# Kernel optimization log

Hardware: AMD Instinct MI355X
Metric: run time of the kernel (lower is better)

The kernel has to match this reference:

```python
import jax, jax.numpy as jnp
import numpy as np

D_MODEL = 2048
N_HEADS = 16
N_KV_HEADS = 4
D_K = D_MODEL // N_HEADS          # 128
N_REP = N_HEADS // N_KV_HEADS     # 4
MAX_SEQ_LEN = 2048


def _rope_tables():
    # Matches torch Rotary: d_k//4 geometric freqs followed by d_k//4 zeros.
    freqs = (1.0 / 10000.0) ** jnp.linspace(0.0, 1.0, D_K // 4, dtype=jnp.float32)
    freqs = jnp.concatenate([freqs, jnp.zeros(D_K // 4, dtype=jnp.float32)])
    t = jnp.arange(MAX_SEQ_LEN, dtype=jnp.float32)
    theta = t[:, None] * freqs[None, :]          # [max_seq_len, d_k//2]
    return jnp.cos(theta), jnp.sin(theta)


def _apply_rotary(x, cos, sin):
    # Faithful to original: x is (B, H, T, D) and the table is indexed by
    # x.size(-3) == H (the original code rotates per-HEAD, broadcast over time).
    H = x.shape[1]
    c = cos[None, :H, None, :]
    s = sin[None, :H, None, :]
    xf = x.astype(jnp.float32)
    x1, x2 = jnp.split(xf, 2, axis=-1)
    y1 = x1 * c + x2 * s
    y2 = -x1 * s + x2 * c
    return jnp.concatenate([y1, y2], axis=-1).astype(x.dtype)


def setup_inputs() -> dict:
    key = jax.random.key(0)
    ks = jax.random.split(key, 5)
    B, T = 2, 2048
    scale = 1.0 / np.sqrt(D_MODEL)
    x = jax.random.normal(ks[0], (B, T, D_MODEL), dtype=jnp.float32)
    wq = jax.random.normal(ks[1], (N_HEADS * D_K, D_MODEL), dtype=jnp.float32) * scale
    wk = jax.random.normal(ks[2], (N_KV_HEADS * D_K, D_MODEL), dtype=jnp.float32) * scale
    wv = jax.random.normal(ks[3], (N_KV_HEADS * D_K, D_MODEL), dtype=jnp.float32) * scale
    wo = jax.random.normal(ks[4], (D_MODEL, D_MODEL), dtype=jnp.float32) * scale
    return {"x": x, "wq": wq, "wk": wk, "wv": wv, "wo": wo}


def reference(x, wq, wk, wv, wo):
    B, T, _ = x.shape
    cos, sin = _rope_tables()

    Q = (x @ wq.T).reshape(B, T, N_HEADS, D_K).transpose(0, 2, 1, 3)      # (B,Hq,T,D)
    K = (x @ wk.T).reshape(B, T, N_KV_HEADS, D_K).transpose(0, 2, 1, 3)   # (B,Hkv,T,D)
    V = (x @ wv.T).reshape(B, T, N_KV_HEADS, D_K).transpose(0, 2, 1, 3)

    Q = _apply_rotary(Q, cos, sin)
    K = _apply_rotary(K, cos, sin)

    # repeat_interleave over head dim to match query heads
    K = jnp.repeat(K, N_REP, axis=1)   # (B,Hq,T,D)
    V = jnp.repeat(V, N_REP, axis=1)

    scale = 1.0 / jnp.sqrt(jnp.asarray(D_K, dtype=jnp.float32))
    scores = jnp.einsum('bhqd,bhkd->bhqk', Q, K) * scale
    causal = jnp.tril(jnp.ones((T, T), dtype=bool))
    scores = jnp.where(causal[None, None, :, :], scores, jnp.finfo(scores.dtype).min)
    attn = jax.nn.softmax(scores, axis=-1)
    out = jnp.einsum('bhqk,bhkd->bhqd', attn, V)          # (B,Hq,T,D)
    out = out.transpose(0, 2, 1, 3).reshape(B, T, D_MODEL)
    return out @ wo.T
```

## Files before the change

kernel.cpp:

```cpp
#include <hip/hip_runtime.h>
#include <cstdint>
#include <cstddef>

typedef __attribute__((ext_vector_type(8))) short bf16x8;
typedef __attribute__((ext_vector_type(4))) float f32x4;
typedef __attribute__((ext_vector_type(16))) float f32x16;
typedef unsigned short ushort_t;

#define MFMA_BF16(a, b, c) __builtin_amdgcn_mfma_f32_16x16x32_bf16((a), (b), (c), 0, 0, 0)
#define MFMA32_BF16(a, b, c) __builtin_amdgcn_mfma_f32_32x32x16_bf16((a), (b), (c), 0, 0, 0)

__device__ __forceinline__ unsigned short f2bf(float f) {
  unsigned int u = __float_as_uint(f);
  u += 0x7fffu + ((u >> 16) & 1u);
  return (unsigned short)(u >> 16);
}
__device__ __forceinline__ float bf2f(unsigned short h) {
  return __uint_as_float(((unsigned int)h) << 16);
}
__device__ __forceinline__ float exp2_fast(float x) {
  float r;
  asm("v_exp_f32 %0, %1" : "=v"(r) : "v"(x));
  return r;
}
__device__ __forceinline__ uint32_t cvtpk_bf16(float lo, float hi) {
  uint32_t r;
  asm("v_cvt_pk_bf16_f32 %0, %1, %2" : "=v"(r) : "v"(lo), "v"(hi));
  return r;
}

__device__ __forceinline__ void gload_lds16(const void* g, void* lds) {
  __builtin_amdgcn_global_load_lds(
      (const __attribute__((address_space(1))) void*)g,
      (__attribute__((address_space(3))) void*)lds, 16, 0, 0);
}

__global__ __launch_bounds__(256)
void cvt_kernel(const float* __restrict__ x, const float* __restrict__ wq,
                const float* __restrict__ wk, const float* __restrict__ wv,
                const float* __restrict__ wo,
                ushort_t* __restrict__ xb, ushort_t* __restrict__ wqb,
                ushort_t* __restrict__ wkb, ushort_t* __restrict__ wvb,
                ushort_t* __restrict__ wob) {
  const float* src; ushort_t* dst; int n;
  switch (blockIdx.y) {
    case 0:  src = x;  dst = xb;  n = 8388608; break;
    case 1:  src = wq; dst = wqb; n = 4194304; break;
    case 2:  src = wk; dst = wkb; n = 1048576; break;
    case 3:  src = wv; dst = wvb; n = 1048576; break;
    default: src = wo; dst = wob; n = 4194304; break;
  }
  const int i = (int)(blockIdx.x * 256u + threadIdx.x) * 4;
  if (i >= n) return;
  const float4 v = *(const float4*)(src + i);
  union { unsigned short us[4]; unsigned long long u64; } pk;
  pk.us[0] = f2bf(v.x); pk.us[1] = f2bf(v.y);
  pk.us[2] = f2bf(v.z); pk.us[3] = f2bf(v.w);
  *(unsigned long long*)(dst + i) = pk.u64;
}

__global__ __launch_bounds__(256, 2)
void gemm_qkv(const ushort_t* __restrict__ A,
              const ushort_t* __restrict__ WQ, const ushort_t* __restrict__ WK,
              const ushort_t* __restrict__ WV,
              ushort_t* __restrict__ Qb, ushort_t* __restrict__ Kb,
              ushort_t* __restrict__ Vtb) {
  __shared__ bf16x8 smem_v[4096];
  char* smem = (char*)smem_v;
  const int tid  = threadIdx.x;
  const int lane = tid & 63;
  const int wave = tid >> 6;
  const int wr = wave >> 1, wc = wave & 1;
  const int y = blockIdx.y;
  int mode, ylocal;
  const ushort_t* Bsel;
  if (y < 16)      { mode = 0; ylocal = y;      Bsel = WQ; }
  else if (y < 20) { mode = 1; ylocal = y - 16; Bsel = WK; }
  else             { mode = 2; ylocal = y - 20; Bsel = WV; }
  const ushort_t* Abase = A + (size_t)blockIdx.x * 128 * 2048;
  const ushort_t* Bbase = Bsel + (size_t)ylocal * 128 * 2048;

  f32x4 acc[4][4] = {};

  #pragma unroll
  for (int it = 0; it < 4; ++it) {
    const int chunk = it * 4 + wave;
    const int r  = chunk * 8 + (lane >> 3);
    const int cg = (lane & 7) ^ (r & 7);
    gload_lds16(Abase + (size_t)r * 2048 + cg * 8, smem + chunk * 1024);
    gload_lds16(Bbase + (size_t)r * 2048 + cg * 8, smem + 16384 + chunk * 1024);
  }
  __syncthreads();

  for (int t = 0; t < 32; ++t) {
    if (t + 1 < 32) {
      char* dst = smem + ((t + 1) & 1) * 32768;
      const int k0 = (t + 1) * 64;
      #pragma unroll
      for (int it = 0; it < 4; ++it) {
        const int chunk = it * 4 + wave;
        const int r  = chunk * 8 + (lane >> 3);
        const int cg = (lane & 7) ^ (r & 7);
        gload_lds16(Abase + (size_t)r * 2048 + k0 + cg * 8, dst + chunk * 1024);
        gload_lds16(Bbase + (size_t)r * 2048 + k0 + cg * 8, dst + 16384 + chunk * 1024);
      }
    }

    char* As = smem + (t & 1) * 32768;
    char* Bs = As + 16384;
    bf16x8 af[2][4], bf_[2][4];
    #pragma unroll
    for (int kki = 0; kki < 2; ++kki) {
      #pragma unroll
      for (int m = 0; m < 4; ++m) {
        const int row = wr * 64 + m * 16 + (lane & 15);
        const int cg  = ((kki << 2) + (lane >> 4)) ^ (row & 7);
        af[kki][m] = *(const bf16x8*)(As + row * 128 + cg * 16);
      }
      #pragma unroll
      for (int n = 0; n < 4; ++n) {
        const int row = wc * 64 + n * 16 + (lane & 15);
        const int cg  = ((kki << 2) + (lane >> 4)) ^ (row & 7);
        bf_[kki][n] = *(const bf16x8*)(Bs + row * 128 + cg * 16);
      }
    }
    #pragma unroll
    for (int kki = 0; kki < 2; ++kki)
      #pragma unroll
      for (int m = 0; m < 4; ++m)
        #pragma unroll
        for (int n = 0; n < 4; ++n)
          acc[m][n] = MFMA_BF16(af[kki][m], bf_[kki][n], acc[m][n]);

    __syncthreads();
  }

  const int row0 = blockIdx.x * 128 + wr * 64;
  const int col0 = ylocal * 128 + wc * 64;
  #pragma unroll
  for (int m = 0; m < 4; ++m) {
    #pragma unroll
    for (int n = 0; n < 4; ++n) {
      #pragma unroll
      for (int j = 0; j < 4; ++j) {
        const int gm = row0 + m * 16 + ((lane >> 4) << 2) + j;
        const int gn = col0 + n * 16 + (lane & 15);
        const float v = acc[m][n][j];
        if (mode == 0) {
          Qb[(size_t)gm * 2048 + gn] = f2bf(v);
        } else if (mode == 1) {
          Kb[(size_t)gm * 512 + gn] = f2bf(v);
        } else {
          const int bb = gm >> 11, t2 = gm & 2047;
          Vtb[(size_t)bb * 512 * 2048 + (size_t)gn * 2048 + t2] = f2bf(v);
        }
      }
    }
  }
}

template<int WMODE>
__global__ __launch_bounds__(256, 2)
void gemm_bt(const ushort_t* __restrict__ A, const ushort_t* __restrict__ B,
             void* __restrict__ Cout, int M, int N, int K) {
  __shared__ bf16x8 smem_v[4096];
  char* smem = (char*)smem_v;
  const int tid  = threadIdx.x;
  const int lane = tid & 63;
  const int wave = tid >> 6;
  const int wr = wave >> 1, wc = wave & 1;
  const ushort_t* Abase = A + (size_t)blockIdx.x * 128 * K;
  const ushort_t* Bbase = B + (size_t)blockIdx.y * 128 * K;

  f32x4 acc[4][4] = {};
  const int nk = K >> 6;

  #pragma unroll
  for (int it = 0; it < 4; ++it) {
    const int chunk = it * 4 + wave;
    const int r  = chunk * 8 + (lane >> 3);
    const int cg = (lane & 7) ^ (r & 7);
    gload_lds16(Abase + (size_t)r * K + cg * 8, smem + chunk * 1024);
    gload_lds16(Bbase + (size_t)r * K + cg * 8, smem + 16384 + chunk * 1024);
  }
  __syncthreads();

  for (int t = 0; t < nk; ++t) {
    if (t + 1 < nk) {
      char* dst = smem + ((t + 1) & 1) * 32768;
      const int k0 = (t + 1) * 64;
      #pragma unroll
      for (int it = 0; it < 4; ++it) {
        const int chunk = it * 4 + wave;
        const int r  = chunk * 8 + (lane >> 3);
        const int cg = (lane & 7) ^ (r & 7);
        gload_lds16(Abase + (size_t)r * K + k0 + cg * 8, dst + chunk * 1024);
        gload_lds16(Bbase + (size_t)r * K + k0 + cg * 8, dst + 16384 + chunk * 1024);
      }
    }

    char* As = smem + (t & 1) * 32768;
    char* Bs = As + 16384;
    bf16x8 af[2][4], bf_[2][4];
    #pragma unroll
    for (int kki = 0; kki < 2; ++kki) {
      #pragma unroll
      for (int m = 0; m < 4; ++m) {
        const int row = wr * 64 + m * 16 + (lane & 15);
        const int cg  = ((kki << 2) + (lane >> 4)) ^ (row & 7);
        af[kki][m] = *(const bf16x8*)(As + row * 128 + cg * 16);
      }
      #pragma unroll
      for (int n = 0; n < 4; ++n) {
        const int row = wc * 64 + n * 16 + (lane & 15);
        const int cg  = ((kki << 2) + (lane >> 4)) ^ (row & 7);
        bf_[kki][n] = *(const bf16x8*)(Bs + row * 128 + cg * 16);
      }
    }
    #pragma unroll
    for (int kki = 0; kki < 2; ++kki)
      #pragma unroll
      for (int m = 0; m < 4; ++m)
        #pragma unroll
        for (int n = 0; n < 4; ++n)
          acc[m][n] = MFMA_BF16(af[kki][m], bf_[kki][n], acc[m][n]);

    __syncthreads();
  }

  const int row0 = blockIdx.x * 128 + wr * 64;
  const int col0 = blockIdx.y * 128 + wc * 64;
  #pragma unroll
  for (int m = 0; m < 4; ++m) {
    #pragma unroll
    for (int n = 0; n < 4; ++n) {
      #pragma unroll
      for (int j = 0; j < 4; ++j) {
        const int gm = row0 + m * 16 + ((lane >> 4) << 2) + j;
        const int gn = col0 + n * 16 + (lane & 15);
        const float v = acc[m][n][j];
        if (WMODE == 0) {
          ((ushort_t*)Cout)[(size_t)gm * N + gn] = f2bf(v);
        } else if (WMODE == 1) {
          ((float*)Cout)[(size_t)gm * N + gn] = v;
        } else {
          const int bb = gm >> 11, t2 = gm & 2047;
          ((ushort_t*)Cout)[(size_t)bb * N * 2048 + (size_t)gn * 2048 + t2] = f2bf(v);
        }
      }
    }
  }
}

__global__ __launch_bounds__(256)
void rope_k_kernel(ushort_t* __restrict__ K) {
  const int idx = blockIdx.x * 256 + threadIdx.x;
  const int NK = 4096 * 4 * 32;
  if (idx >= NK) return;
  const int t = idx >> 7, r = idx & 127;
  const int h = r >> 5, i = r & 31;
  ushort_t* p = K + (size_t)t * 512 + h * 128;
  const float f  = powf(10000.0f, -(float)i / 31.0f);
  const float th = (float)h * f;
  float sn, cs;
  sincosf(th, &sn, &cs);
  const float x1 = bf2f(p[i]), x2 = bf2f(p[i + 64]);
  p[i]      = f2bf(x1 * cs + x2 * sn);
  p[i + 64] = f2bf(-x1 * sn + x2 * cs);
}

__global__ __launch_bounds__(256, 2)
void attn_kernel(const ushort_t* __restrict__ Q, const ushort_t* __restrict__ K,
                 const ushort_t* __restrict__ Vt, ushort_t* __restrict__ AO) {
  __shared__ bf16x8 smem_v[4096];
  char* smem = (char*)smem_v;
  const int tid  = threadIdx.x;
  const int lane = tid & 63;
  const int wq   = tid >> 6;
  const int ql   = lane & 31;
  const int hi   = lane >> 5;
  const int h  = blockIdx.y;
  const int b  = blockIdx.z;
  const int qt = (b == 0) ? ((int)gridDim.x - 1 - (int)blockIdx.x)
                          : (int)blockIdx.x;
  const int kh = h >> 2;
  const int q0b = qt * 128;
  const int qmin_w = q0b + wq * 32;
  const int qmax_w = qmin_w + 31;
  const int qrow = qmin_w + ql;

  const ushort_t* Qp = Q  + (size_t)b * 2048 * 2048 + (size_t)h  * 128;
  const ushort_t* Kp = K  + (size_t)b * 2048 * 512  + (size_t)kh * 128;
  const ushort_t* Vp = Vt + (size_t)b * 512 * 2048  + (size_t)kh * 128 * 2048;

  const int ntiles = (qt + 1) * 2;

  #pragma unroll
  for (int it = 0; it < 4; ++it) {
    const int ck = it * 4 + wq;
    const int rK = ck * 4 + (lane >> 4);
    const int gK = (lane & 15) ^ (rK & 7);
    gload_lds16(Kp + (size_t)rK * 512 + gK * 8, smem + ck * 1024);
    const int rV = ck * 8 + (lane >> 3);
    const int gV = (lane & 7) ^ (rV & 7);
    gload_lds16(Vp + (size_t)rV * 2048 + gV * 8, smem + 16384 + ck * 1024);
  }

  const float SCL = 0.08838834764831845f * 1.4426950408889634f;
  bf16x8 qf[8];
  #pragma unroll
  for (int ks = 0; ks < 8; ++ks)
    qf[ks] = *(const bf16x8*)(Qp + (size_t)qrow * 2048 + ks * 16 + hi * 8);
  #pragma unroll
  for (int ks = 0; ks < 2; ++ks) {
    union { bf16x8 v; ushort_t us[8]; } X1, X2;
    X1.v = qf[ks]; X2.v = qf[ks + 4];
    #pragma unroll
    for (int e = 0; e < 8; ++e) {
      const int i = ks * 16 + hi * 8 + e;
      const float f = __expf(-(float)i * (9.2103403720f / 31.0f));
      float sn, cs;
      sincosf((float)h * f, &sn, &cs);
      const float x1 = bf2f(X1.us[e]), x2 = bf2f(X2.us[e]);
      X1.us[e] = f2bf((x1 * cs + x2 * sn) * SCL);
      X2.us[e] = f2bf((-x1 * sn + x2 * cs) * SCL);
    }
    qf[ks] = X1.v; qf[ks + 4] = X2.v;
  }
  #pragma unroll
  for (int ks = 2; ks < 4; ++ks) {
    union { bf16x8 v; ushort_t us[8]; } X1, X2;
    X1.v = qf[ks]; X2.v = qf[ks + 4];
    #pragma unroll
    for (int e = 0; e < 8; ++e) {
      X1.us[e] = f2bf(bf2f(X1.us[e]) * SCL);
      X2.us[e] = f2bf(bf2f(X2.us[e]) * SCL);
    }
    qf[ks] = X1.v; qf[ks + 4] = X2.v;
  }

  float m_ = -3.0e38f, l_ = 0.f;
  f32x16 oacc[4] = {};

  __syncthreads();

  for (int ti = 0; ti < ntiles; ++ti) {
    const int kv0 = ti * 64;
    if (ti + 1 < ntiles) {
      const int nkv0 = kv0 + 64;
      char* dst = smem + ((ti + 1) & 1) * 32768;
      #pragma unroll
      for (int it = 0; it < 4; ++it) {
        const int ck = it * 4 + wq;
        const int rK = ck * 4 + (lane >> 4);
        const int gK = (lane & 15) ^ (rK & 7);
        gload_lds16(Kp + (size_t)(nkv0 + rK) * 512 + gK * 8, dst + ck * 1024);
        const int rV = ck * 8 + (lane >> 3);
        const int gV = (lane & 7) ^ (rV & 7);
        gload_lds16(Vp + (size_t)rV * 2048 + nkv0 + gV * 8, dst + 16384 + ck * 1024);
      }
    }

    char* Ks = smem + (ti & 1) * 32768;
    char* Vs = Ks + 16384;
    if (kv0 <= qmax_w) {
      f32x16 sacc[2] = {};
      __builtin_amdgcn_s_setprio(1);
      #pragma unroll
      for (int kg = 0; kg < 2; ++kg) {
        const int key = kg * 32 + ql;
        #pragma unroll
        for (int ks = 0; ks < 8; ++ks) {
          const int g = ((ks << 1) + hi) ^ (key & 7);
          const bf16x8 kf = *(const bf16x8*)(Ks + key * 256 + g * 16);
          sacc[kg] = MFMA32_BF16(kf, qf[ks], sacc[kg]);
        }
      }
      __builtin_amdgcn_s_setprio(0);

      if (kv0 + 63 > qmin_w) {
        #pragma unroll
        for (int kg = 0; kg < 2; ++kg)
          #pragma unroll
          for (int r = 0; r < 16; ++r) {
            const int keyg = kv0 + kg * 32 + (r & 3) + 8 * (r >> 2) + 4 * hi;
            if (keyg > qrow) sacc[kg][r] = -3.0e38f;
          }
      }

      float mx[8];
      #pragma unroll
      for (int i = 0; i < 8; ++i) {
        const int kg = i >> 2, base = (i & 3) * 4;
        mx[i] = fmaxf(fmaxf(sacc[kg][base], sacc[kg][base + 1]),
                      fmaxf(sacc[kg][base + 2], sacc[kg][base + 3]));
      }
      float pm = fmaxf(fmaxf(fmaxf(mx[0], mx[1]), fmaxf(mx[2], mx[3])),
                       fmaxf(fmaxf(mx[4], mx[5]), fmaxf(mx[6], mx[7])));
      pm = fmaxf(pm, __shfl_xor(pm, 32));

      if (__any(pm > m_ + 11.0f)) {
        const float mn = fmaxf(m_, pm);
        const float alpha = exp2_fast(m_ - mn);
        m_ = mn;
        l_ *= alpha;
        #pragma unroll
        for (int r = 0; r < 16; ++r) {
          const float ar = __shfl(alpha, (r & 3) + 8 * (r >> 2) + 4 * hi);
          #pragma unroll
          for (int dg = 0; dg < 4; ++dg) oacc[dg][r] *= ar;
        }
      }

      float rs0 = 0.f, rs1 = 0.f, rs2 = 0.f, rs3 = 0.f;
      #pragma unroll
      for (int kg = 0; kg < 2; ++kg)
        #pragma unroll
        for (int r = 0; r < 16; r += 4) {
          const float p0 = exp2_fast(sacc[kg][r]     - m_);
          const float p1 = exp2_fast(sacc[kg][r + 1] - m_);
          const float p2 = exp2_fast(sacc[kg][r + 2] - m_);
          const float p3 = exp2_fast(sacc[kg][r + 3] - m_);
          sacc[kg][r] = p0; sacc[kg][r + 1] = p1;
          sacc[kg][r + 2] = p2; sacc[kg][r + 3] = p3;
          rs0 += p0; rs1 += p1; rs2 += p2; rs3 += p3;
        }
      float rs = (rs0 + rs1) + (rs2 + rs3);
      rs += __shfl_xor(rs, 32);
      l_ += rs;

      bf16x8 pa[4];
      #pragma unroll
      for (int ks = 0; ks < 4; ++ks) {
        const int kg = ks >> 1;
        const int base = 8 * (ks & 1);
        union { uint32_t w[4]; bf16x8 v; } U;
        #pragma unroll
        for (int j = 0; j < 2; ++j) {
          uint32_t a  = cvtpk_bf16(sacc[kg][base + 2 * j],     sacc[kg][base + 2 * j + 1]);
          uint32_t bb = cvtpk_bf16(sacc[kg][base + 4 + 2 * j], sacc[kg][base + 4 + 2 * j + 1]);
          asm volatile("v_permlane32_swap_b32 %0, %1" : "+v"(a), "+v"(bb));
          U.w[j] = a; U.w[2 + j] = bb;
        }
        pa[ks] = U.v;
      }

      __builtin_amdgcn_s_setprio(1);
      #pragma unroll
      for (int dg = 0; dg < 4; ++dg) {
        const int d = dg * 32 + ql;
        #pragma unroll
        for (int ks = 0; ks < 4; ++ks) {
          const int g = ((ks << 1) + hi) ^ (d & 7);
          const bf16x8 vf = *(const bf16x8*)(Vs + d * 128 + g * 16);
          oacc[dg] = MFMA32_BF16(pa[ks], vf, oacc[dg]);
        }
      }
      __builtin_amdgcn_s_setprio(0);
    }

    __syncthreads();
  }

  const float linv = 1.0f / l_;
  ushort_t* AOp = AO + (size_t)b * 2048 * 2048 + (size_t)h * 128;
  #pragma unroll
  for (int r = 0; r < 16; ++r) {
    const int cr = (r & 3) + 8 * (r >> 2) + 4 * hi;
    const float li = __shfl(linv, cr);
    const int row = q0b + wq * 32 + cr;
    #pragma unroll
    for (int dg = 0; dg < 4; ++dg)
      AOp[(size_t)row * 2048 + dg * 32 + ql] = f2bf(oacc[dg][r] * li);
  }
}

extern "C" void kernel_launch(void* const* d_in, const int* in_sizes, int n_in,
                              void* d_out, int out_size, void* d_ws, size_t ws_size,
                              hipStream_t stream) {
  const float* x  = (const float*)d_in[0];
  const float* wq = (const float*)d_in[1];
  const float* wk = (const float*)d_in[2];
  const float* wv = (const float*)d_in[3];
  const float* wo = (const float*)d_in[4];
  float* out = (float*)d_out;
  char* ws = (char*)d_ws;

  ushort_t* xb  = (ushort_t*)(ws);
  ushort_t* wqb = (ushort_t*)(ws + 16777216);
  ushort_t* wkb = (ushort_t*)(ws + 25165824);
  ushort_t* wvb = (ushort_t*)(ws + 27262976);
  ushort_t* wob = (ushort_t*)(ws + 29360128);
  ushort_t* Qb  = (ushort_t*)(ws + 37748736);
  ushort_t* Kb  = (ushort_t*)(ws + 54525952);
  ushort_t* Vtb = (ushort_t*)(ws + 58720256);
  ushort_t* AOb = (ushort_t*)(ws + 62914560);

  cvt_kernel<<<dim3(8192, 5), 256, 0, stream>>>(x, wq, wk, wv, wo,
                                                xb, wqb, wkb, wvb, wob);
  gemm_qkv<<<dim3(32, 24), 256, 0, stream>>>(xb, wqb, wkb, wvb, Qb, Kb, Vtb);
  rope_k_kernel<<<dim3(2048), 256, 0, stream>>>(Kb);
  attn_kernel<<<dim3(16, 16, 2), 256, 0, stream>>>(Qb, Kb, Vtb, AOb);
  gemm_bt<1><<<dim3(32, 16), 256, 0, stream>>>(AOb, wob, out, 4096, 2048, 2048);
}
```

Measured before the change: 189.9 us.

## Halve QKV GEMM K-tile for higher occupancy and remap attention blocks per XCD

The QKV projection GEMM now stages 32-wide K slices instead of 64. This halves its shared memory to 32 KB and allows 3 blocks per CU, with a new swizzle matched to the narrower rows. The cost is twice as many loop iterations and barriers. Separately, the attention grid index is remapped so blocks that share a KV head and batch land on the same XCD, aiming for better L2 reuse of K/V. The remap also pairs causal query tiles (qt and 15-qt) for load balance.

```diff
diff --git a/kernel.cpp b/kernel.cpp
--- a/kernel.cpp
+++ b/kernel.cpp
@@ -59,13 +59,13 @@
   *(unsigned long long*)(dst + i) = pk.u64;
 }
 
-__global__ __launch_bounds__(256, 2)
+__global__ __launch_bounds__(256, 3)
 void gemm_qkv(const ushort_t* __restrict__ A,
               const ushort_t* __restrict__ WQ, const ushort_t* __restrict__ WK,
               const ushort_t* __restrict__ WV,
               ushort_t* __restrict__ Qb, ushort_t* __restrict__ Kb,
               ushort_t* __restrict__ Vtb) {
-  __shared__ bf16x8 smem_v[4096];
+  __shared__ bf16x8 smem_v[2048];
   char* smem = (char*)smem_v;
   const int tid  = threadIdx.x;
   const int lane = tid & 63;
@@ -82,58 +82,52 @@
 
   f32x4 acc[4][4] = {};
 
-  #pragma unroll
-  for (int it = 0; it < 4; ++it) {
-    const int chunk = it * 4 + wave;
-    const int r  = chunk * 8 + (lane >> 3);
-    const int cg = (lane & 7) ^ (r & 7);
-    gload_lds16(Abase + (size_t)r * 2048 + cg * 8, smem + chunk * 1024);
-    gload_lds16(Bbase + (size_t)r * 2048 + cg * 8, smem + 16384 + chunk * 1024);
-  }
+#define QKV_STAGE(T, BUF)                                                    \
+  {                                                                          \
+    const int k0_ = (T) * 32;                                                \
+    _Pragma("unroll")                                                        \
+    for (int it = 0; it < 2; ++it) {                                         \
+      const int c = it * 4 + wave;                                           \
+      const int row = c * 16 + (lane >> 2);                                  \
+      const int gs = (lane & 3) ^ ((row >> 1) & 3);                          \
+      gload_lds16(Abase + (size_t)row * 2048 + k0_ + gs * 8, (BUF) + c * 1024);       \
+      gload_lds16(Bbase + (size_t)row * 2048 + k0_ + gs * 8, (BUF) + 8192 + c * 1024);\
+    }                                                                        \
+  }
+
+  QKV_STAGE(0, smem);
   __syncthreads();
 
-  for (int t = 0; t < 32; ++t) {
-    if (t + 1 < 32) {
-      char* dst = smem + ((t + 1) & 1) * 32768;
-      const int k0 = (t + 1) * 64;
-      #pragma unroll
-      for (int it = 0; it < 4; ++it) {
-        const int chunk = it * 4 + wave;
-        const int r  = chunk * 8 + (lane >> 3);
-        const int cg = (lane & 7) ^ (r & 7);
-        gload_lds16(Abase + (size_t)r * 2048 + k0 + cg * 8, dst + chunk * 1024);
-        gload_lds16(Bbase + (size_t)r * 2048 + k0 + cg * 8, dst + 16384 + chunk * 1024);
-      }
-    }
-
-    char* As = smem + (t & 1) * 32768;
-    char* Bs = As + 16384;
-    bf16x8 af[2][4], bf_[2][4];
-    #pragma unroll
-    for (int kki = 0; kki < 2; ++kki) {
-      #pragma unroll
-      for (int m = 0; m < 4; ++m) {
-        const int row = wr * 64 + m * 16 + (lane & 15);
-        const int cg  = ((kki << 2) + (lane >> 4)) ^ (row & 7);
-        af[kki][m] = *(const bf16x8*)(As + row * 128 + cg * 16);
-      }
-      #pragma unroll
-      for (int n = 0; n < 4; ++n) {
-        const int row = wc * 64 + n * 16 + (lane & 15);
-        const int cg  = ((kki << 2) + (lane >> 4)) ^ (row & 7);
-        bf_[kki][n] = *(const bf16x8*)(Bs + row * 128 + cg * 16);
-      }
-    }
-    #pragma unroll
-    for (int kki = 0; kki < 2; ++kki)
-      #pragma unroll
-      for (int m = 0; m < 4; ++m)
-        #pragma unroll
-        for (int n = 0; n < 4; ++n)
-          acc[m][n] = MFMA_BF16(af[kki][m], bf_[kki][n], acc[m][n]);
+  for (int t = 0; t < 64; ++t) {
+    if (t + 1 < 64) {
+      char* dst = smem + ((t + 1) & 1) * 16384;
+      QKV_STAGE(t + 1, dst);
+    }
+
+    char* As = smem + (t & 1) * 16384;
+    char* Bs = As + 8192;
+    bf16x8 af[4], bf_[4];
+    #pragma unroll
+    for (int m = 0; m < 4; ++m) {
+      const int row = wr * 64 + m * 16 + (lane & 15);
+      const int g = (lane >> 4) ^ ((row >> 1) & 3);
+      af[m] = *(const bf16x8*)(As + row * 64 + g * 16);
+    }
+    #pragma unroll
+    for (int n = 0; n < 4; ++n) {
+      const int row = wc * 64 + n * 16 + (lane & 15);
+      const int g = (lane >> 4) ^ ((row >> 1) & 3);
+      bf_[n] = *(const bf16x8*)(Bs + row * 64 + g * 16);
+    }
+    #pragma unroll
+    for (int m = 0; m < 4; ++m)
+      #pragma unroll
+      for (int n = 0; n < 4; ++n)
+        acc[m][n] = MFMA_BF16(af[m], bf_[n], acc[m][n]);
 
     __syncthreads();
   }
+#undef QKV_STAGE
 
   const int row0 = blockIdx.x * 128 + wr * 64;
   const int col0 = ylocal * 128 + wc * 64;
@@ -279,11 +273,16 @@
   const int wq   = tid >> 6;
   const int ql   = lane & 31;
   const int hi   = lane >> 5;
-  const int h  = blockIdx.y;
-  const int b  = blockIdx.z;
-  const int qt = (b == 0) ? ((int)gridDim.x - 1 - (int)blockIdx.x)
-                          : (int)blockIdx.x;
-  const int kh = h >> 2;
+
+  const int lin = (int)blockIdx.x + 16 * (int)blockIdx.y + 256 * (int)blockIdx.z;
+  const int xcd = lin & 7;
+  const int s   = lin >> 3;
+  const int b   = xcd >> 2;
+  const int kh  = xcd & 3;
+  const int h   = (kh << 2) + (s & 3);
+  const int s4  = s >> 2;
+  const int qt  = (s4 < 8) ? s4 : (23 - s4);
+
   const int q0b = qt * 128;
   const int qmin_w = q0b + wq * 32;
   const int qmax_w = qmin_w + 31;
```

After: 191.0 us. No clear change (+0.6%).

## Remap attention blocks per XCD, stage only K in LDS, read V from global

Applied to the files above, without the earlier changes.

Recomputes the block-to-work mapping so each XCD handles one (batch, KV-head) pair, keeping the shared K/V in that XCD's L2. Query tiles are folded to balance causal work. LDS now double-buffers two 64-key K sub-tiles (128 keys per sync) instead of one K+V tile. V fragments are loaded directly from global memory into registers inside the PV MFMA loop. This halves the barriers and frees LDS bandwidth, at the cost of global-load latency in the PV step.

```diff
diff --git a/kernel.cpp b/kernel.cpp
--- a/kernel.cpp
+++ b/kernel.cpp
@@ -279,11 +279,16 @@
   const int wq   = tid >> 6;
   const int ql   = lane & 31;
   const int hi   = lane >> 5;
-  const int h  = blockIdx.y;
-  const int b  = blockIdx.z;
-  const int qt = (b == 0) ? ((int)gridDim.x - 1 - (int)blockIdx.x)
-                          : (int)blockIdx.x;
-  const int kh = h >> 2;
+
+  const int lin = (int)blockIdx.x + 16 * (int)blockIdx.y + 256 * (int)blockIdx.z;
+  const int xcd = lin & 7;
+  const int s   = lin >> 3;
+  const int b   = xcd >> 2;
+  const int kh  = xcd & 3;
+  const int h   = (kh << 2) + (s & 3);
+  const int s4  = s >> 2;
+  const int qt  = (s4 < 8) ? s4 : (23 - s4);
+
   const int q0b = qt * 128;
   const int qmin_w = q0b + wq * 32;
   const int qmax_w = qmin_w + 31;
@@ -293,18 +298,24 @@
   const ushort_t* Kp = K  + (size_t)b * 2048 * 512  + (size_t)kh * 128;
   const ushort_t* Vp = Vt + (size_t)b * 512 * 2048  + (size_t)kh * 128 * 2048;
 
-  const int ntiles = (qt + 1) * 2;
-
-  #pragma unroll
-  for (int it = 0; it < 4; ++it) {
-    const int ck = it * 4 + wq;
-    const int rK = ck * 4 + (lane >> 4);
-    const int gK = (lane & 15) ^ (rK & 7);
-    gload_lds16(Kp + (size_t)rK * 512 + gK * 8, smem + ck * 1024);
-    const int rV = ck * 8 + (lane >> 3);
-    const int gV = (lane & 7) ^ (rV & 7);
-    gload_lds16(Vp + (size_t)rV * 2048 + gV * 8, smem + 16384 + ck * 1024);
-  }
+  const int nint = qt + 1;
+
+#define K_STAGE(KV0, BUF)                                                    \
+  {                                                                          \
+    _Pragma("unroll")                                                        \
+    for (int sb = 0; sb < 2; ++sb) {                                         \
+      _Pragma("unroll")                                                      \
+      for (int it = 0; it < 4; ++it) {                                       \
+        const int ck = it * 4 + wq;                                          \
+        const int rK = ck * 4 + (lane >> 4);                                 \
+        const int gK = (lane & 15) ^ (rK & 7);                               \
+        gload_lds16(Kp + (size_t)((KV0) + sb * 64 + rK) * 512 + gK * 8,      \
+                    (BUF) + sb * 16384 + ck * 1024);                         \
+      }                                                                      \
+    }                                                                        \
+  }
+
+  K_STAGE(0, smem);
 
   const float SCL = 0.08838834764831845f * 1.4426950408889634f;
   bf16x8 qf[8];
@@ -344,123 +355,116 @@
 
   __syncthreads();
 
-  for (int ti = 0; ti < ntiles; ++ti) {
-    const int kv0 = ti * 64;
-    if (ti + 1 < ntiles) {
-      const int nkv0 = kv0 + 64;
+  for (int ti = 0; ti < nint; ++ti) {
+    if (ti + 1 < nint) {
       char* dst = smem + ((ti + 1) & 1) * 32768;
-      #pragma unroll
-      for (int it = 0; it < 4; ++it) {
-        const int ck = it * 4 + wq;
-        const int rK = ck * 4 + (lane >> 4);
-        const int gK = (lane & 15) ^ (rK & 7);
-        gload_lds16(Kp + (size_t)(nkv0 + rK) * 512 + gK * 8, dst + ck * 1024);
-        const int rV = ck * 8 + (lane >> 3);
-        const int gV = (lane & 7) ^ (rV & 7);
-        gload_lds16(Vp + (size_t)rV * 2048 + nkv0 + gV * 8, dst + 16384 + ck * 1024);
-      }
-    }
-
-    char* Ks = smem + (ti & 1) * 32768;
-    char* Vs = Ks + 16384;
-    if (kv0 <= qmax_w) {
-      f32x16 sacc[2] = {};
-      __builtin_amdgcn_s_setprio(1);
-      #pragma unroll
-      for (int kg = 0; kg < 2; ++kg) {
-        const int key = kg * 32 + ql;
-        #pragma unroll
-        for (int ks = 0; ks < 8; ++ks) {
-          const int g = ((ks << 1) + hi) ^ (key & 7);
-          const bf16x8 kf = *(const bf16x8*)(Ks + key * 256 + g * 16);
-          sacc[kg] = MFMA32_BF16(kf, qf[ks], sacc[kg]);
-        }
-      }
-      __builtin_amdgcn_s_setprio(0);
-
-      if (kv0 + 63 > qmin_w) {
+      K_STAGE((ti + 1) * 128, dst);
+    }
+    char* bufK = smem + (ti & 1) * 32768;
+
+    #pragma unroll
+    for (int sb = 0; sb < 2; ++sb) {
+      const int kvs = ti * 128 + sb * 64;
+      char* Ks = bufK + sb * 16384;
+      if (kvs <= qmax_w) {
+        f32x16 sacc[2] = {};
+        __builtin_amdgcn_s_setprio(1);
+        #pragma unroll
+        for (int kg = 0; kg < 2; ++kg) {
+          const int key = kg * 32 + ql;
+          #pragma unroll
+          for (int ks = 0; ks < 8; ++ks) {
+            const int g = ((ks << 1) + hi) ^ (key & 7);
+            const bf16x8 kf = *(const bf16x8*)(Ks + key * 256 + g * 16);
+            sacc[kg] = MFMA32_BF16(kf, qf[ks], sacc[kg]);
+          }
+        }
+        __builtin_amdgcn_s_setprio(0);
+
+        if (kvs + 63 > qmin_w) {
+          #pragma unroll
+          for (int kg = 0; kg < 2; ++kg)
+            #pragma unroll
+            for (int r = 0; r < 16; ++r) {
+              const int keyg = kvs + kg * 32 + (r & 3) + 8 * (r >> 2) + 4 * hi;
+              if (keyg > qrow) sacc[kg][r] = -3.0e38f;
+            }
+        }
+
+        float mx[8];
+        #pragma unroll
+        for (int i = 0; i < 8; ++i) {
+          const int kg = i >> 2, base = (i & 3) * 4;
+          mx[i] = fmaxf(fmaxf(sacc[kg][base], sacc[kg][base + 1]),
+                        fmaxf(sacc[kg][base + 2], sacc[kg][base + 3]));
+        }
+        float pm = fmaxf(fmaxf(fmaxf(mx[0], mx[1]), fmaxf(mx[2], mx[3])),
+                         fmaxf(fmaxf(mx[4], mx[5]), fmaxf(mx[6], mx[7])));
+        pm = fmaxf(pm, __shfl_xor(pm, 32));
+
+        if (__any(pm > m_ + 11.0f)) {
+          const float mn = fmaxf(m_, pm);
+          const float alpha = exp2_fast(m_ - mn);
+          m_ = mn;
+          l_ *= alpha;
+          #pragma unroll
+          for (int r = 0; r < 16; ++r) {
+            const float ar = __shfl(alpha, (r & 3) + 8 * (r >> 2) + 4 * hi);
+            #pragma unroll
+            for (int dg = 0; dg < 4; ++dg) oacc[dg][r] *= ar;
+          }
+        }
+
+        float rs0 = 0.f, rs1 = 0.f, rs2 = 0.f, rs3 = 0.f;
         #pragma unroll
         for (int kg = 0; kg < 2; ++kg)
           #pragma unroll
-          for (int r = 0; r < 16; ++r) {
-            const int keyg = kv0 + kg * 32 + (r & 3) + 8 * (r >> 2) + 4 * hi;
-            if (keyg > qrow) sacc[kg][r] = -3.0e38f;
+          for (int r = 0; r < 16; r += 4) {
+            const float p0 = exp2_fast(sacc[kg][r]     - m_);
+            const float p1 = exp2_fast(sacc[kg][r + 1] - m_);
+            const float p2 = exp2_fast(sacc[kg][r + 2] - m_);
+            const float p3 = exp2_fast(sacc[kg][r + 3] - m_);
+            sacc[kg][r] = p0; sacc[kg][r + 1] = p1;
+            sacc[kg][r + 2] = p2; sacc[kg][r + 3] = p3;
+            rs0 += p0; rs1 += p1; rs2 += p2; rs3 += p3;
           }
-      }
-
-      float mx[8];
-      #pragma unroll
-      for (int i = 0; i < 8; ++i) {
-        const int kg = i >> 2, base = (i & 3) * 4;
-        mx[i] = fmaxf(fmaxf(sacc[kg][base], sacc[kg][base + 1]),
-                      fmaxf(sacc[kg][base + 2], sacc[kg][base + 3]));
-      }
-      float pm = fmaxf(fmaxf(fmaxf(mx[0], mx[1]), fmaxf(mx[2], mx[3])),
-                       fmaxf(fmaxf(mx[4], mx[5]), fmaxf(mx[6], mx[7])));
-      pm = fmaxf(pm, __shfl_xor(pm, 32));
-
-      if (__any(pm > m_ + 11.0f)) {
-        const float mn = fmaxf(m_, pm);
-        const float alpha = exp2_fast(m_ - mn);
-        m_ = mn;
-        l_ *= alpha;
-        #pragma unroll
-        for (int r = 0; r < 16; ++r) {
-          const float ar = __shfl(alpha, (r & 3) + 8 * (r >> 2) + 4 * hi);
+        float rs = (rs0 + rs1) + (rs2 + rs3);
+        rs += __shfl_xor(rs, 32);
+        l_ += rs;
+
+        bf16x8 pa[4];
+        #pragma unroll
+        for (int ks = 0; ks < 4; ++ks) {
+          const int kg = ks >> 1;
+          const int base = 8 * (ks & 1);
+          union { uint32_t w[4]; bf16x8 v; } U;
           #pragma unroll
-          for (int dg = 0; dg < 4; ++dg) oacc[dg][r] *= ar;
-        }
-      }
-
-      float rs0 = 0.f, rs1 = 0.f, rs2 = 0.f, rs3 = 0.f;
-      #pragma unroll
-      for (int kg = 0; kg < 2; ++kg)
-        #pragma unroll
-        for (int r = 0; r < 16; r += 4) {
-          const float p0 = exp2_fast(sacc[kg][r]     - m_);
-          const float p1 = exp2_fast(sacc[kg][r + 1] - m_);
-          const float p2 = exp2_fast(sacc[kg][r + 2] - m_);
-          const float p3 = exp2_fast(sacc[kg][r + 3] - m_);
-          sacc[kg][r] = p0; sacc[kg][r + 1] = p1;
-          sacc[kg][r + 2] = p2; sacc[kg][r + 3] = p3;
-          rs0 += p0; rs1 += p1; rs2 += p2; rs3 += p3;
-        }
-      float rs = (rs0 + rs1) + (rs2 + rs3);
-      rs += __shfl_xor(rs, 32);
-      l_ += rs;
-
-      bf16x8 pa[4];
-      #pragma unroll
-      for (int ks = 0; ks < 4; ++ks) {
-        const int kg = ks >> 1;
-        const int base = 8 * (ks & 1);
-        union { uint32_t w[4]; bf16x8 v; } U;
-        #pragma unroll
-        for (int j = 0; j < 2; ++j) {
-          uint32_t a  = cvtpk_bf16(sacc[kg][base + 2 * j],     sacc[kg][base + 2 * j + 1]);
-          uint32_t bb = cvtpk_bf16(sacc[kg][base + 4 + 2 * j], sacc[kg][base + 4 + 2 * j + 1]);
-          asm volatile("v_permlane32_swap_b32 %0, %1" : "+v"(a), "+v"(bb));
-          U.w[j] = a; U.w[2 + j] = bb;
-        }
-        pa[ks] = U.v;
-      }
-
-      __builtin_amdgcn_s_setprio(1);
-      #pragma unroll
-      for (int dg = 0; dg < 4; ++dg) {
-        const int d = dg * 32 + ql;
-        #pragma unroll
-        for (int ks = 0; ks < 4; ++ks) {
-          const int g = ((ks << 1) + hi) ^ (d & 7);
-          const bf16x8 vf = *(const bf16x8*)(Vs + d * 128 + g * 16);
-          oacc[dg] = MFMA32_BF16(pa[ks], vf, oacc[dg]);
-        }
-      }
-      __builtin_amdgcn_s_setprio(0);
+          for (int j = 0; j < 2; ++j) {
+            uint32_t a  = cvtpk_bf16(sacc[kg][base + 2 * j],     sacc[kg][base + 2 * j + 1]);
+            uint32_t bb = cvtpk_bf16(sacc[kg][base + 4 + 2 * j], sacc[kg][base + 4 + 2 * j + 1]);
+            asm volatile("v_permlane32_swap_b32 %0, %1" : "+v"(a), "+v"(bb));
+            U.w[j] = a; U.w[2 + j] = bb;
+          }
+          pa[ks] = U.v;
+        }
+
+        __builtin_amdgcn_s_setprio(1);
+        #pragma unroll
+        for (int dg = 0; dg < 4; ++dg) {
+          const ushort_t* vrow = Vp + (size_t)(dg * 32 + ql) * 2048 + kvs + hi * 8;
+          #pragma unroll
+          for (int ks = 0; ks < 4; ++ks) {
+            const bf16x8 vf = *(const bf16x8*)(vrow + ks * 16);
+            oacc[dg] = MFMA32_BF16(pa[ks], vf, oacc[dg]);
+          }
+        }
+        __builtin_amdgcn_s_setprio(0);
+      }
     }
 
     __syncthreads();
   }
+#undef K_STAGE
 
   const float linv = 1.0f / l_;
   ushort_t* AOp = AO + (size_t)b * 2048 * 2048 + (size_t)h * 128;
```

Result: slower. 239.0 us (+25.8%).

## Split causal attention KV range across two blocks and merge partial results

Applied to the files above, without the earlier changes.

Each 128-row query tile's key/value range is now split into two halves handled by separate blocks. This doubles the grid and evens out the causal-mask load imbalance. Each half writes a partial bf16 output plus its running max and sum, and a new combine kernel rescales and merges the two partials. Block indices are also remapped so blocks sharing a KV head and batch land on the same XCD, to improve L2 reuse. The cost is an extra kernel launch, extra global traffic for the partial outputs, and an extra bf16 rounding step on the partials.

```diff
diff --git a/kernel.cpp b/kernel.cpp
--- a/kernel.cpp
+++ b/kernel.cpp
@@ -271,7 +271,9 @@
 
 __global__ __launch_bounds__(256, 2)
 void attn_kernel(const ushort_t* __restrict__ Q, const ushort_t* __restrict__ K,
-                 const ushort_t* __restrict__ Vt, ushort_t* __restrict__ AO) {
+                 const ushort_t* __restrict__ Vt,
+                 ushort_t* __restrict__ AO0, ushort_t* __restrict__ AO1,
+                 float* __restrict__ ml) {
   __shared__ bf16x8 smem_v[4096];
   char* smem = (char*)smem_v;
   const int tid  = threadIdx.x;
@@ -279,11 +281,17 @@
   const int wq   = tid >> 6;
   const int ql   = lane & 31;
   const int hi   = lane >> 5;
-  const int h  = blockIdx.y;
-  const int b  = blockIdx.z;
-  const int qt = (b == 0) ? ((int)gridDim.x - 1 - (int)blockIdx.x)
-                          : (int)blockIdx.x;
-  const int kh = h >> 2;
+
+  const int lin = (int)blockIdx.x + 32 * (int)blockIdx.y + 512 * (int)blockIdx.z;
+  const int xcd = lin & 7;
+  const int s   = lin >> 3;
+  const int b   = xcd >> 2;
+  const int kh  = xcd & 3;
+  const int h   = (kh << 2) + (s & 3);
+  const int rest = s >> 2;
+  const int qt   = 15 - (rest >> 1);
+  const int half = rest & 1;
+
   const int q0b = qt * 128;
   const int qmin_w = q0b + wq * 32;
   const int qmax_w = qmin_w + 31;
@@ -293,17 +301,21 @@
   const ushort_t* Kp = K  + (size_t)b * 2048 * 512  + (size_t)kh * 128;
   const ushort_t* Vp = Vt + (size_t)b * 512 * 2048  + (size_t)kh * 128 * 2048;
 
-  const int ntiles = (qt + 1) * 2;
-
-  #pragma unroll
-  for (int it = 0; it < 4; ++it) {
-    const int ck = it * 4 + wq;
-    const int rK = ck * 4 + (lane >> 4);
-    const int gK = (lane & 15) ^ (rK & 7);
-    gload_lds16(Kp + (size_t)rK * 512 + gK * 8, smem + ck * 1024);
-    const int rV = ck * 8 + (lane >> 3);
-    const int gV = (lane & 7) ^ (rV & 7);
-    gload_lds16(Vp + (size_t)rV * 2048 + gV * 8, smem + 16384 + ck * 1024);
+  const int nt   = qt + 1;
+  const int tbase = half * nt;
+
+  {
+    const int kv0 = tbase * 64;
+    #pragma unroll
+    for (int it = 0; it < 4; ++it) {
+      const int ck = it * 4 + wq;
+      const int rK = ck * 4 + (lane >> 4);
+      const int gK = (lane & 15) ^ (rK & 7);
+      gload_lds16(Kp + (size_t)(kv0 + rK) * 512 + gK * 8, smem + ck * 1024);
+      const int rV = ck * 8 + (lane >> 3);
+      const int gV = (lane & 7) ^ (rV & 7);
+      gload_lds16(Vp + (size_t)rV * 2048 + kv0 + gV * 8, smem + 16384 + ck * 1024);
+    }
   }
 
   const float SCL = 0.08838834764831845f * 1.4426950408889634f;
@@ -344,9 +356,9 @@
 
   __syncthreads();
 
-  for (int ti = 0; ti < ntiles; ++ti) {
-    const int kv0 = ti * 64;
-    if (ti + 1 < ntiles) {
+  for (int ti = 0; ti < nt; ++ti) {
+    const int kv0 = (tbase + ti) * 64;
+    if (ti + 1 < nt) {
       const int nkv0 = kv0 + 64;
       char* dst = smem + ((ti + 1) & 1) * 32768;
       #pragma unroll
@@ -462,8 +474,8 @@
     __syncthreads();
   }
 
-  const float linv = 1.0f / l_;
-  ushort_t* AOp = AO + (size_t)b * 2048 * 2048 + (size_t)h * 128;
+  const float linv = (l_ > 0.f) ? (1.0f / l_) : 0.f;
+  ushort_t* AOp = (half ? AO1 : AO0) + (size_t)b * 2048 * 2048 + (size_t)h * 128;
   #pragma unroll
   for (int r = 0; r < 16; ++r) {
     const int cr = (r & 3) + 8 * (r >> 2) + 4 * hi;
@@ -473,6 +485,34 @@
     for (int dg = 0; dg < 4; ++dg)
       AOp[(size_t)row * 2048 + dg * 32 + ql] = f2bf(oacc[dg][r] * li);
   }
+  if (hi == 0) {
+    float* mlp = ml + ((((size_t)b * 16 + h) * 2048 + qrow) * 4 + half * 2);
+    mlp[0] = m_;
+    mlp[1] = l_;
+  }
+}
+
+__global__ __launch_bounds__(256)
+void combine_kernel(ushort_t* __restrict__ AO0, const ushort_t* __restrict__ AO1,
+                    const float* __restrict__ ml) {
+  const size_t i8 = ((size_t)blockIdx.x * 256 + threadIdx.x) * 8;
+  const int b = (int)(i8 >> 22);
+  const int r = (int)(i8 & 4194303);
+  const int t = r >> 11;
+  const int h = (r & 2047) >> 7;
+  const float4 m4 = *(const float4*)(ml + (((size_t)b * 16 + h) * 2048 + t) * 4);
+  const float M  = fmaxf(m4.x, m4.z);
+  const float u0 = m4.y * exp2_fast(m4.x - M);
+  const float u1 = m4.w * exp2_fast(m4.z - M);
+  const float inv = 1.0f / (u0 + u1);
+  const float w0 = u0 * inv, w1 = u1 * inv;
+  union { bf16x8 v; ushort_t us[8]; } A, B, O;
+  A.v = *(const bf16x8*)(AO0 + i8);
+  B.v = *(const bf16x8*)(AO1 + i8);
+  #pragma unroll
+  for (int j = 0; j < 8; ++j)
+    O.us[j] = f2bf(w0 * bf2f(A.us[j]) + w1 * bf2f(B.us[j]));
+  *(bf16x8*)(AO0 + i8) = O.v;
 }
 
 extern "C" void kernel_launch(void* const* d_in, const int* in_sizes, int n_in,
@@ -494,12 +534,15 @@
   ushort_t* Qb  = (ushort_t*)(ws + 37748736);
   ushort_t* Kb  = (ushort_t*)(ws + 54525952);
   ushort_t* Vtb = (ushort_t*)(ws + 58720256);
-  ushort_t* AOb = (ushort_t*)(ws + 62914560);
+  ushort_t* AO0 = (ushort_t*)(ws + 62914560);
+  ushort_t* AO1 = (ushort_t*)(ws);
+  float*    ml  = (float*)(ws + 16777216);
 
   cvt_kernel<<<dim3(8192, 5), 256, 0, stream>>>(x, wq, wk, wv, wo,
                                                 xb, wqb, wkb, wvb, wob);
   gemm_qkv<<<dim3(32, 24), 256, 0, stream>>>(xb, wqb, wkb, wvb, Qb, Kb, Vtb);
   rope_k_kernel<<<dim3(2048), 256, 0, stream>>>(Kb);
-  attn_kernel<<<dim3(16, 16, 2), 256, 0, stream>>>(Qb, Kb, Vtb, AOb);
-  gemm_bt<1><<<dim3(32, 16), 256, 0, stream>>>(AOb, wob, out, 4096, 2048, 2048);
-}
+  attn_kernel<<<dim3(32, 16, 2), 256, 0, stream>>>(Qb, Kb, Vtb, AO0, AO1, ml);
+  combine_kernel<<<dim3(4096), 256, 0, stream>>>(AO0, AO1, ml);
+  gemm_bt<1><<<dim3(32, 16), 256, 0, stream>>>(AO0, wob, out, 4096, 2048, 2048);
+}
```

After: 196.3 us. +3.3%, slower.
